# Kernel optimization log

Measured on AMD Instinct MI355X. Metric: run time of the kernel, lower is better.

## Reference

```python
import jax, jax.numpy as jnp
import numpy as np

NEG_SLOPE = 0.01  # torch F.leaky_relu default


def setup_inputs() -> dict:
    key = jax.random.key(0)
    k1, k2, k3, k4, k5 = jax.random.split(key, 5)
    N, E, IN_DIM, OUT_DIM = 100000, 1600000, 128, 64
    h = jax.random.normal(k1, (N, IN_DIM), dtype=jnp.float32)
    src = jax.random.randint(k2, (E,), 0, N, dtype=jnp.int64)
    dst = jax.random.randint(k3, (E,), 0, N, dtype=jnp.int64)
    # xavier_normal-ish scaled params
    W1 = jax.random.normal(k4, (OUT_DIM, IN_DIM), dtype=jnp.float32) * (2.0 / (IN_DIM + OUT_DIM)) ** 0.5
    Wa = jax.random.normal(k5, (1, 2 * OUT_DIM), dtype=jnp.float32) * (2.0 / (2 * OUT_DIM + 1)) ** 0.5
    return {"h": h, "src": src, "dst": dst, "W1": W1, "Wa": Wa}


def reference(h, src, dst, W1, Wa):
    N = h.shape[0]
    D = W1.shape[0]
    z = h @ W1.T  # [N, D]
    z_src = z[src]  # [E, D] gather
    z_dst = z[dst]  # [E, D] gather
    a_src, a_dst = Wa[0, :D], Wa[0, D:]
    # attn_fc(concat(z_src, z_dst)) == z_src@a_src + z_dst@a_dst
    e = z_src @ a_src + z_dst @ a_dst  # [E]
    e = jnp.where(e >= 0, e, NEG_SLOPE * e)  # leaky_relu
    # segment softmax over incoming edges of each dst node
    e_max = jax.ops.segment_max(e, dst, num_segments=N)
    e_max = jnp.where(jnp.isfinite(e_max), e_max, 0.0)  # empty segments
    e_exp = jnp.exp(e - e_max[dst])
    denom = jax.ops.segment_sum(e_exp, dst, num_segments=N)
    alpha = e_exp / jnp.maximum(denom, 1e-16)[dst]  # [E]
    # weighted scatter-sum of source messages
    h_out = jax.ops.segment_sum(alpha[:, None] * z_src, dst, num_segments=N)  # [N, D]
    return h_out
```

## Files before the change

### kernel.cpp

```cpp
#include <hip/hip_runtime.h>
#include <hip/hip_bf16.h>

#define NEG_SLOPE 0.01f
#define NPB 512
#define CHUNK 4096

typedef __attribute__((ext_vector_type(8))) short short8;
typedef __attribute__((ext_vector_type(4))) float f32x4;

__device__ __forceinline__ unsigned short f2bf_rne(float f) {
    unsigned u = __float_as_uint(f);
    u += 0x7FFFu + ((u >> 16) & 1u);
    return (unsigned short)(u >> 16);
}

__global__ __launch_bounds__(256, 4) void k_gp(
    const float* __restrict__ h, const float* __restrict__ W1,
    const float* __restrict__ Wa, unsigned short* __restrict__ zb,
    float* __restrict__ s, float* __restrict__ t, int N, int G1,
    const int* __restrict__ src, const int* __restrict__ dst,
    unsigned* __restrict__ gcur, unsigned* __restrict__ table,
    int E, int NBKT, int BCAP)
{
    __shared__ __align__(16) union SM {
        struct { short wsb[64 * 128]; short tbuf[4][16 * 64]; } g;
        struct {
            unsigned cnt[256]; unsigned exc[256]; unsigned sbuf[256];
            unsigned gbaseb[256]; unsigned stage[CHUNK];
            unsigned short bkt[CHUNK];
        } p;
    } sm;
    const int tid = threadIdx.x;

    if (blockIdx.x < (unsigned)G1) {
        const int nb = blockIdx.x * 256;
        const int w  = tid >> 6;
        const int l  = tid & 63;
        const int lr = l & 15;
        const int lc = l >> 4;
        const int rowbase = nb + w * 64;
        const float4* __restrict__ h4 = (const float4*)h;
        const float4* __restrict__ W14 = (const float4*)W1;

        float asrc[4], adst[4];
#pragma unroll
        for (int ni = 0; ni < 4; ++ni) {
            asrc[ni] = Wa[ni * 16 + lr];
            adst[ni] = Wa[64 + ni * 16 + lr];
        }

        float4 av[8];
        {
            const int myn = rowbase + lr;
#pragma unroll
            for (int ks = 0; ks < 4; ++ks) {
                const int kcb = ks * 4 + lc;
                if (myn < N) {
                    av[2 * ks]     = h4[(size_t)myn * 32 + kcb * 2];
                    av[2 * ks + 1] = h4[(size_t)myn * 32 + kcb * 2 + 1];
                } else {
                    av[2 * ks]     = make_float4(0.f, 0.f, 0.f, 0.f);
                    av[2 * ks + 1] = make_float4(0.f, 0.f, 0.f, 0.f);
                }
            }
        }

#pragma unroll
        for (int it = 0; it < 4; ++it) {
            const int q = tid + it * 256;
            const int r = q >> 4, cb = q & 15;
            float4 v0 = W14[(size_t)r * 32 + cb * 2];
            float4 v1 = W14[(size_t)r * 32 + cb * 2 + 1];
            short8 o;
            o[0]=f2bf_rne(v0.x); o[1]=f2bf_rne(v0.y); o[2]=f2bf_rne(v0.z); o[3]=f2bf_rne(v0.w);
            o[4]=f2bf_rne(v1.x); o[5]=f2bf_rne(v1.y); o[6]=f2bf_rne(v1.z); o[7]=f2bf_rne(v1.w);
            *(short8*)&sm.g.wsb[r * 128 + ((cb * 8) ^ ((r & 7) << 3))] = o;
        }
        __syncthreads();

        short* __restrict__ tb = sm.g.tbuf[w];

#pragma unroll
        for (int rg = 0; rg < 4; ++rg) {
            short8 afr[4];
#pragma unroll
            for (int ks = 0; ks < 4; ++ks) {
                const float4 v0 = av[2 * ks], v1 = av[2 * ks + 1];
                short8 o;
                o[0]=f2bf_rne(v0.x); o[1]=f2bf_rne(v0.y); o[2]=f2bf_rne(v0.z); o[3]=f2bf_rne(v0.w);
                o[4]=f2bf_rne(v1.x); o[5]=f2bf_rne(v1.y); o[6]=f2bf_rne(v1.z); o[7]=f2bf_rne(v1.w);
                afr[ks] = o;
            }
            if (rg < 3) {
                const int myn = rowbase + (rg + 1) * 16 + lr;
#pragma unroll
                for (int ks = 0; ks < 4; ++ks) {
                    const int kcb = ks * 4 + lc;
                    if (myn < N) {
                        av[2 * ks]     = h4[(size_t)myn * 32 + kcb * 2];
                        av[2 * ks + 1] = h4[(size_t)myn * 32 + kcb * 2 + 1];
                    } else {
                        av[2 * ks]     = make_float4(0.f, 0.f, 0.f, 0.f);
                        av[2 * ks + 1] = make_float4(0.f, 0.f, 0.f, 0.f);
                    }
                }
            }

            f32x4 acc[4];
#pragma unroll
            for (int ni = 0; ni < 4; ++ni) acc[ni] = (f32x4){0.f, 0.f, 0.f, 0.f};
#pragma unroll
            for (int ks = 0; ks < 4; ++ks) {
                const int kcb = ks * 4 + lc;
#pragma unroll
                for (int ni = 0; ni < 4; ++ni) {
                    const int wr = ni * 16 + lr;
                    const short8 bf = *(const short8*)&sm.g.wsb[wr * 128 + ((kcb * 8) ^ ((wr & 7) << 3))];
                    acc[ni] = __builtin_amdgcn_mfma_f32_16x16x32_bf16(afr[ks], bf, acc[ni], 0, 0, 0);
                }
            }

#pragma unroll
            for (int r = 0; r < 4; ++r) {
                float ps = 0.f, pt = 0.f;
#pragma unroll
                for (int ni = 0; ni < 4; ++ni) {
                    ps = fmaf(acc[ni][r], asrc[ni], ps);
                    pt = fmaf(acc[ni][r], adst[ni], pt);
                }
#pragma unroll
                for (int m = 1; m < 16; m <<= 1) {
                    ps += __shfl_xor(ps, m);
                    pt += __shfl_xor(pt, m);
                }
                const int node = rowbase + rg * 16 + lc * 4 + r;
                if (lr == 0 && node < N) { s[node] = ps; t[node] = pt; }
            }

#pragma unroll
            for (int ni = 0; ni < 4; ++ni) {
                const int col = ni * 16 + lr;
#pragma unroll
                for (int r = 0; r < 4; ++r) {
                    const int ro = lc * 4 + r;
                    tb[ro * 64 + (((col >> 3) ^ (ro & 7)) << 3) + (col & 7)]
                        = (short)f2bf_rne(acc[ni][r]);
                }
            }
            {
                const int ro = l >> 2;
                const int n = rowbase + rg * 16 + ro;
                if (n < N) {
#pragma unroll
                    for (int j = 0; j < 2; ++j) {
                        const int c = (l & 3) * 2 + j;
                        const short8 v = *(const short8*)&tb[ro * 64 + ((c ^ (ro & 7)) << 3)];
                        *(short8*)&zb[(size_t)n * 64 + c * 8] = v;
                    }
                }
            }
        }
    } else {
        const int e0 = (blockIdx.x - G1) * CHUNK;
        const int nE = min(CHUNK, E - e0);

        sm.p.cnt[tid] = 0u;
        __syncthreads();
        for (int i = tid; i < nE; i += 256)
            atomicAdd(&sm.p.cnt[(unsigned)dst[e0 + i] >> 9], 1u);
        __syncthreads();

        const unsigned myc = sm.p.cnt[tid];
        if (tid < NBKT && myc > 0u) sm.p.gbaseb[tid] = atomicAdd(&gcur[tid], myc);

        sm.p.sbuf[tid] = myc;
        __syncthreads();
        for (int off = 1; off < 256; off <<= 1) {
            unsigned x = (tid >= off) ? sm.p.sbuf[tid - off] : 0u;
            __syncthreads();
            sm.p.sbuf[tid] += x;
            __syncthreads();
        }
        sm.p.exc[tid] = sm.p.sbuf[tid] - myc;
        __syncthreads();
        sm.p.cnt[tid] = 0u;
        __syncthreads();

        for (int i = tid; i < nE; i += 256) {
            const unsigned d = (unsigned)dst[e0 + i];
            const unsigned b = d >> 9;
            const unsigned pos = sm.p.exc[b] + atomicAdd(&sm.p.cnt[b], 1u);
            sm.p.stage[pos] = ((unsigned)src[e0 + i] << 9) | (d & 511u);
            sm.p.bkt[pos] = (unsigned short)b;
        }
        __syncthreads();

        for (int i = tid; i < nE; i += 256) {
            const unsigned b = sm.p.bkt[i];
            const unsigned off = sm.p.gbaseb[b] + ((unsigned)i - sm.p.exc[b]);
            if (off < (unsigned)BCAP)
                table[(size_t)b * BCAP + off] = sm.p.stage[i];
        }
    }
}

__global__ __launch_bounds__(512) void k_sp(
    const unsigned* __restrict__ table, const unsigned* __restrict__ gcur,
    const float* __restrict__ s, const float* __restrict__ t,
    uint2* __restrict__ edge_ps, unsigned* __restrict__ offsets,
    unsigned* __restrict__ counts, float* __restrict__ invden,
    int N, int NBKT, int BCAP)
{
    __shared__ unsigned ncnt[NPB], nexc[NPB], scur[NPB], sbuf[NPB];
    __shared__ float tlds[NPB], den[NPB];
    __shared__ unsigned basesh;
    const int tid = threadIdx.x;
    const int b = blockIdx.x;
    const int bc = min((int)gcur[b], BCAP);
    const size_t tbo = (size_t)b * BCAP;
    const int node = b * NPB + tid;

    {
        unsigned c = (tid < NBKT) ? min(gcur[tid], (unsigned)BCAP) : 0u;
        sbuf[tid] = c;
        __syncthreads();
        for (int off = 1; off < NPB; off <<= 1) {
            unsigned x = (tid >= off) ? sbuf[tid - off] : 0u;
            __syncthreads();
            sbuf[tid] += x;
            __syncthreads();
        }
        if (tid == 0) basesh = (b == 0) ? 0u : sbuf[b - 1];
    }
    tlds[tid] = (node < N) ? t[node] : 0.f;
    den[tid] = 0.f;
    ncnt[tid] = 0u;
    __syncthreads();
    const unsigned base = basesh;

    for (int i = tid; i < bc; i += NPB)
        atomicAdd(&ncnt[table[tbo + i] & 511u], 1u);
    __syncthreads();

    const unsigned c0 = ncnt[tid];
    sbuf[tid] = c0;
    __syncthreads();
    for (int off = 1; off < NPB; off <<= 1) {
        unsigned x = (tid >= off) ? sbuf[tid - off] : 0u;
        __syncthreads();
        sbuf[tid] += x;
        __syncthreads();
    }
    nexc[tid] = sbuf[tid] - c0;
    scur[tid] = 0u;
    __syncthreads();

    if (node < N) { offsets[node] = base + nexc[tid]; counts[node] = c0; }

    for (int i = tid; i < bc; i += NPB) {
        const unsigned v = table[tbo + i];
        const unsigned l = v & 511u;
        const unsigned sj = v >> 9;
        float e = s[sj] + tlds[l];
        e = (e >= 0.f) ? e : NEG_SLOPE * e;
        const float p = __expf(e);
        const unsigned pos = nexc[l] + atomicAdd(&scur[l], 1u);
        edge_ps[base + pos] = make_uint2(__float_as_uint(p), sj);
        atomicAdd(&den[l], p);
    }
    __syncthreads();
    if (node < N) invden[node] = 1.f / fmaxf(den[tid], 1e-16f);
}

__global__ __launch_bounds__(256) void k_node(
    const unsigned* __restrict__ offsets, const unsigned* __restrict__ counts,
    const uint2* __restrict__ edge_ps, const float* __restrict__ invden,
    const unsigned short* __restrict__ zb, float* __restrict__ out, int N)
{
    const int tid = threadIdx.x;
    const int node = blockIdx.x * 16 + (tid >> 4);
    if (node >= N) return;
    const int wl    = tid & 63;
    const int gbase = wl & ~15;
    const int sub   = wl & 15;
    const int g2    = sub >> 3;
    const int l8    = sub & 7;

    const unsigned beg = offsets[node];
    const int cnt = (int)counts[node];
    if (cnt == 0) {
        if (sub < 8) {
            const float4 zz = make_float4(0.f, 0.f, 0.f, 0.f);
            *(float4*)&out[(size_t)node * 64 + sub * 8]     = zz;
            *(float4*)&out[(size_t)node * 64 + sub * 8 + 4] = zz;
        }
        return;
    }

    const float invd = invden[node];
    const unsigned short* __restrict__ zrow = zb + l8 * 8;
    float acc[8] = {0.f, 0.f, 0.f, 0.f, 0.f, 0.f, 0.f, 0.f};

    for (int base = 0; base < cnt; base += 16) {
        const int rem = cnt - base;
        uint2 ep = make_uint2(0u, 0u);
        if (sub < rem) ep = edge_ps[beg + base + sub];
        const float p = __uint_as_float(ep.x);
        const int  sj = (int)ep.y;

        uint4 vv[8];
#pragma unroll
        for (int k = 0; k < 8; ++k) {
            const int sjj = __shfl(sj, gbase + g2 * 8 + k);
            vv[k] = *(const uint4*)&zrow[(size_t)sjj * 64];
        }
#pragma unroll
        for (int k = 0; k < 8; ++k) {
            const float pj = __shfl(p, gbase + g2 * 8 + k);
            const uint4 v = vv[k];
#define UNPK(u, d0) \
            acc[d0]     = fmaf(pj, __uint_as_float((u) << 16),          acc[d0]); \
            acc[d0 + 1] = fmaf(pj, __uint_as_float((u) & 0xFFFF0000u), acc[d0 + 1]);
            UNPK(v.x, 0) UNPK(v.y, 2) UNPK(v.z, 4) UNPK(v.w, 6)
#undef UNPK
        }
    }

#pragma unroll
    for (int c = 0; c < 8; ++c)
        acc[c] += __shfl_xor(acc[c], 8);

    if (sub < 8) {
        float4 o0 = make_float4(acc[0] * invd, acc[1] * invd, acc[2] * invd, acc[3] * invd);
        float4 o1 = make_float4(acc[4] * invd, acc[5] * invd, acc[6] * invd, acc[7] * invd);
        *(float4*)&out[(size_t)node * 64 + sub * 8]     = o0;
        *(float4*)&out[(size_t)node * 64 + sub * 8 + 4] = o1;
    }
}

extern "C" void kernel_launch(void* const* d_in, const int* in_sizes, int n_in,
                              void* d_out, int out_size, void* d_ws, size_t ws_size,
                              hipStream_t stream) {
    const float* h   = (const float*)d_in[0];
    const int*   src = (const int*)d_in[1];
    const int*   dst = (const int*)d_in[2];
    const float* W1  = (const float*)d_in[3];
    const float* Wa  = (const float*)d_in[4];
    float* out = (float*)d_out;

    const int N = in_sizes[0] / 128;
    const int E = in_sizes[1];
    const int NBKT = (N + NPB - 1) / NPB;
    const int meanb = (E + NBKT - 1) / NBKT;
    int slack = 24 * (int)sqrtf((float)meanb) + 64;
    const int BCAP = meanb + slack;

    const int G1 = (N + 255) / 256;
    const int G2 = (E + CHUNK - 1) / CHUNK;

    unsigned short* zb = (unsigned short*)d_ws;
    float*    s        = (float*)(zb + (size_t)N * 64);
    float*    t        = s + N;
    unsigned* gcur     = (unsigned*)(t + N);
    unsigned* offsets  = gcur + NBKT;
    unsigned* counts   = offsets + N;
    float*    invden   = (float*)(counts + N);
    uint2*    edge_ps  = (uint2*)(invden + N);
    unsigned* table    = (unsigned*)(edge_ps + E);

    hipMemsetAsync(gcur, 0, (size_t)NBKT * sizeof(unsigned), stream);

    k_gp<<<G1 + G2, 256, 0, stream>>>(h, W1, Wa, zb, s, t, N, G1,
                                      src, dst, gcur, table, E, NBKT, BCAP);
    k_sp<<<NBKT, 512, 0, stream>>>(table, gcur, s, t, edge_ps, offsets, counts,
                                   invden, N, NBKT, BCAP);
    k_node<<<(N + 15) / 16, 256, 0, stream>>>(offsets, counts, edge_ps, invden, zb, out, N);
}
```

Before: 95.19 us.

## Fuse softmax and node aggregation into one kernel with LDS edge lists

Merges the per-bucket softmax kernel and the per-node aggregation kernel into one kernel. Each block handles a quarter of a 512-node bucket and keeps the sorted (p, src) edge list in shared memory, so the global edge_ps, offsets, counts and invden buffers and one launch go away. The cost is that every quarter-block rescans the whole bucket table (four times the table reads), and edges past QCAP are silently dropped. The bf16 conversion also switches to the library intrinsic, and the global prefix scan over buckets is no longer needed.

```diff
diff --git a/kernel.cpp b/kernel.cpp
--- a/kernel.cpp
+++ b/kernel.cpp
@@ -3,15 +3,35 @@
 
 #define NEG_SLOPE 0.01f
 #define NPB 512
+#define QN  128
+#define QCAP 2600
 #define CHUNK 4096
 
 typedef __attribute__((ext_vector_type(8))) short short8;
 typedef __attribute__((ext_vector_type(4))) float f32x4;
 
 __device__ __forceinline__ unsigned short f2bf_rne(float f) {
-    unsigned u = __float_as_uint(f);
-    u += 0x7FFFu + ((u >> 16) & 1u);
-    return (unsigned short)(u >> 16);
+    __hip_bfloat16 b = __float2bfloat16(f);
+    return __builtin_bit_cast(unsigned short, b);
+}
+
+__device__ __forceinline__ short8 cvt2(float4 v0, float4 v1) {
+    short8 o;
+    o[0]=(short)f2bf_rne(v0.x); o[1]=(short)f2bf_rne(v0.y);
+    o[2]=(short)f2bf_rne(v0.z); o[3]=(short)f2bf_rne(v0.w);
+    o[4]=(short)f2bf_rne(v1.x); o[5]=(short)f2bf_rne(v1.y);
+    o[6]=(short)f2bf_rne(v1.z); o[7]=(short)f2bf_rne(v1.w);
+    return o;
+}
+
+__device__ __forceinline__ unsigned wscan_incl(unsigned v) {
+    const int ln = threadIdx.x & 63;
+#pragma unroll
+    for (int off = 1; off < 64; off <<= 1) {
+        unsigned x = __shfl_up(v, off);
+        if (ln >= off) v += x;
+    }
+    return v;
 }
 
 __global__ __launch_bounds__(256, 4) void k_gp(
@@ -71,10 +91,7 @@
             const int r = q >> 4, cb = q & 15;
             float4 v0 = W14[(size_t)r * 32 + cb * 2];
             float4 v1 = W14[(size_t)r * 32 + cb * 2 + 1];
-            short8 o;
-            o[0]=f2bf_rne(v0.x); o[1]=f2bf_rne(v0.y); o[2]=f2bf_rne(v0.z); o[3]=f2bf_rne(v0.w);
-            o[4]=f2bf_rne(v1.x); o[5]=f2bf_rne(v1.y); o[6]=f2bf_rne(v1.z); o[7]=f2bf_rne(v1.w);
-            *(short8*)&sm.g.wsb[r * 128 + ((cb * 8) ^ ((r & 7) << 3))] = o;
+            *(short8*)&sm.g.wsb[r * 128 + ((cb * 8) ^ ((r & 7) << 3))] = cvt2(v0, v1);
         }
         __syncthreads();
 
@@ -84,13 +101,7 @@
         for (int rg = 0; rg < 4; ++rg) {
             short8 afr[4];
 #pragma unroll
-            for (int ks = 0; ks < 4; ++ks) {
-                const float4 v0 = av[2 * ks], v1 = av[2 * ks + 1];
-                short8 o;
-                o[0]=f2bf_rne(v0.x); o[1]=f2bf_rne(v0.y); o[2]=f2bf_rne(v0.z); o[3]=f2bf_rne(v0.w);
-                o[4]=f2bf_rne(v1.x); o[5]=f2bf_rne(v1.y); o[6]=f2bf_rne(v1.z); o[7]=f2bf_rne(v1.w);
-                afr[ks] = o;
-            }
+            for (int ks = 0; ks < 4; ++ks) afr[ks] = cvt2(av[2 * ks], av[2 * ks + 1]);
             if (rg < 3) {
                 const int myn = rowbase + (rg + 1) * 16 + lr;
 #pragma unroll
@@ -204,137 +215,117 @@
     }
 }
 
-__global__ __launch_bounds__(512) void k_sp(
+__global__ __launch_bounds__(256) void k_sn(
     const unsigned* __restrict__ table, const unsigned* __restrict__ gcur,
     const float* __restrict__ s, const float* __restrict__ t,
-    uint2* __restrict__ edge_ps, unsigned* __restrict__ offsets,
-    unsigned* __restrict__ counts, float* __restrict__ invden,
-    int N, int NBKT, int BCAP)
+    const unsigned short* __restrict__ zb, float* __restrict__ out,
+    int N, int BCAP)
 {
-    __shared__ unsigned ncnt[NPB], nexc[NPB], scur[NPB], sbuf[NPB];
-    __shared__ float tlds[NPB], den[NPB];
-    __shared__ unsigned basesh;
+    __shared__ unsigned ncnt[QN], nexc[QN], scur[QN];
+    __shared__ float tl[QN], den[QN], invd[QN];
+    __shared__ unsigned wtot[2];
+    __shared__ __align__(8) uint2 elist[QCAP];
+
     const int tid = threadIdx.x;
-    const int b = blockIdx.x;
+    const int b  = blockIdx.x >> 2;
+    const int qr = blockIdx.x & 3;
+    const int node0 = b * NPB + qr * QN;
     const int bc = min((int)gcur[b], BCAP);
     const size_t tbo = (size_t)b * BCAP;
-    const int node = b * NPB + tid;
-
-    {
-        unsigned c = (tid < NBKT) ? min(gcur[tid], (unsigned)BCAP) : 0u;
-        sbuf[tid] = c;
-        __syncthreads();
-        for (int off = 1; off < NPB; off <<= 1) {
-            unsigned x = (tid >= off) ? sbuf[tid - off] : 0u;
-            __syncthreads();
-            sbuf[tid] += x;
-            __syncthreads();
-        }
-        if (tid == 0) basesh = (b == 0) ? 0u : sbuf[b - 1];
-    }
-    tlds[tid] = (node < N) ? t[node] : 0.f;
-    den[tid] = 0.f;
-    ncnt[tid] = 0u;
-    __syncthreads();
-    const unsigned base = basesh;
-
-    for (int i = tid; i < bc; i += NPB)
-        atomicAdd(&ncnt[table[tbo + i] & 511u], 1u);
-    __syncthreads();
-
-    const unsigned c0 = ncnt[tid];
-    sbuf[tid] = c0;
-    __syncthreads();
-    for (int off = 1; off < NPB; off <<= 1) {
-        unsigned x = (tid >= off) ? sbuf[tid - off] : 0u;
-        __syncthreads();
-        sbuf[tid] += x;
-        __syncthreads();
-    }
-    nexc[tid] = sbuf[tid] - c0;
-    scur[tid] = 0u;
-    __syncthreads();
-
-    if (node < N) { offsets[node] = base + nexc[tid]; counts[node] = c0; }
-
-    for (int i = tid; i < bc; i += NPB) {
+
+    if (tid < QN) {
+        ncnt[tid] = 0u; scur[tid] = 0u; den[tid] = 0.f;
+        const int n = node0 + tid;
+        tl[tid] = (n < N) ? t[n] : 0.f;
+    }
+    __syncthreads();
+
+    for (int i = tid; i < bc; i += 256) {
         const unsigned v = table[tbo + i];
-        const unsigned l = v & 511u;
+        if (((v >> 7) & 3u) == (unsigned)qr)
+            atomicAdd(&ncnt[v & 127u], 1u);
+    }
+    __syncthreads();
+
+    if (tid < QN) {
+        const unsigned c = ncnt[tid];
+        const unsigned inc = wscan_incl(c);
+        if ((tid & 63) == 63) wtot[tid >> 6] = inc;
+        nexc[tid] = inc - c;
+    }
+    __syncthreads();
+    if (tid >= 64 && tid < QN) nexc[tid] += wtot[0];
+    __syncthreads();
+
+    for (int i = tid; i < bc; i += 256) {
+        const unsigned v = table[tbo + i];
+        if (((v >> 7) & 3u) != (unsigned)qr) continue;
+        const unsigned l = v & 127u;
         const unsigned sj = v >> 9;
-        float e = s[sj] + tlds[l];
+        float e = s[sj] + tl[l];
         e = (e >= 0.f) ? e : NEG_SLOPE * e;
         const float p = __expf(e);
         const unsigned pos = nexc[l] + atomicAdd(&scur[l], 1u);
-        edge_ps[base + pos] = make_uint2(__float_as_uint(p), sj);
-        atomicAdd(&den[l], p);
-    }
-    __syncthreads();
-    if (node < N) invden[node] = 1.f / fmaxf(den[tid], 1e-16f);
-}
-
-__global__ __launch_bounds__(256) void k_node(
-    const unsigned* __restrict__ offsets, const unsigned* __restrict__ counts,
-    const uint2* __restrict__ edge_ps, const float* __restrict__ invden,
-    const unsigned short* __restrict__ zb, float* __restrict__ out, int N)
-{
-    const int tid = threadIdx.x;
-    const int node = blockIdx.x * 16 + (tid >> 4);
-    if (node >= N) return;
+        if (pos < (unsigned)QCAP) {
+            elist[pos] = make_uint2(__float_as_uint(p), sj);
+            atomicAdd(&den[l], p);
+        }
+    }
+    __syncthreads();
+    if (tid < QN) invd[tid] = 1.f / fmaxf(den[tid], 1e-16f);
+    __syncthreads();
+
     const int wl    = tid & 63;
+    const int w     = tid >> 6;
     const int gbase = wl & ~15;
     const int sub   = wl & 15;
     const int g2    = sub >> 3;
     const int l8    = sub & 7;
-
-    const unsigned beg = offsets[node];
-    const int cnt = (int)counts[node];
-    if (cnt == 0) {
-        if (sub < 8) {
-            const float4 zz = make_float4(0.f, 0.f, 0.f, 0.f);
-            *(float4*)&out[(size_t)node * 64 + sub * 8]     = zz;
-            *(float4*)&out[(size_t)node * 64 + sub * 8 + 4] = zz;
-        }
-        return;
-    }
-
-    const float invd = invden[node];
     const unsigned short* __restrict__ zrow = zb + l8 * 8;
-    float acc[8] = {0.f, 0.f, 0.f, 0.f, 0.f, 0.f, 0.f, 0.f};
-
-    for (int base = 0; base < cnt; base += 16) {
-        const int rem = cnt - base;
-        uint2 ep = make_uint2(0u, 0u);
-        if (sub < rem) ep = edge_ps[beg + base + sub];
-        const float p = __uint_as_float(ep.x);
-        const int  sj = (int)ep.y;
-
-        uint4 vv[8];
-#pragma unroll
-        for (int k = 0; k < 8; ++k) {
-            const int sjj = __shfl(sj, gbase + g2 * 8 + k);
-            vv[k] = *(const uint4*)&zrow[(size_t)sjj * 64];
-        }
-#pragma unroll
-        for (int k = 0; k < 8; ++k) {
-            const float pj = __shfl(p, gbase + g2 * 8 + k);
-            const uint4 v = vv[k];
+
+    for (int grp = 0; grp < 8; ++grp) {
+        const int l  = grp * 16 + w * 4 + (wl >> 4);
+        const int gn = node0 + l;
+        const unsigned beg = nexc[l];
+        const int cnt = (int)ncnt[l];
+
+        float acc[8] = {0.f, 0.f, 0.f, 0.f, 0.f, 0.f, 0.f, 0.f};
+        for (int base = 0; base < cnt; base += 16) {
+            const int rem = cnt - base;
+            uint2 ep = make_uint2(0u, 0u);
+            if (sub < rem) ep = elist[beg + base + sub];
+            const float p = __uint_as_float(ep.x);
+            const int  sj = (int)ep.y;
+
+            uint4 vv[8];
+#pragma unroll
+            for (int k = 0; k < 8; ++k) {
+                const int sjj = __shfl(sj, gbase + g2 * 8 + k);
+                vv[k] = *(const uint4*)&zrow[(size_t)sjj * 64];
+            }
+#pragma unroll
+            for (int k = 0; k < 8; ++k) {
+                const float pj = __shfl(p, gbase + g2 * 8 + k);
+                const uint4 v = vv[k];
 #define UNPK(u, d0) \
-            acc[d0]     = fmaf(pj, __uint_as_float((u) << 16),          acc[d0]); \
-            acc[d0 + 1] = fmaf(pj, __uint_as_float((u) & 0xFFFF0000u), acc[d0 + 1]);
-            UNPK(v.x, 0) UNPK(v.y, 2) UNPK(v.z, 4) UNPK(v.w, 6)
+                acc[d0]     = fmaf(pj, __uint_as_float((u) << 16),          acc[d0]); \
+                acc[d0 + 1] = fmaf(pj, __uint_as_float((u) & 0xFFFF0000u), acc[d0 + 1]);
+                UNPK(v.x, 0) UNPK(v.y, 2) UNPK(v.z, 4) UNPK(v.w, 6)
 #undef UNPK
-        }
-    }
-
-#pragma unroll
-    for (int c = 0; c < 8; ++c)
-        acc[c] += __shfl_xor(acc[c], 8);
-
-    if (sub < 8) {
-        float4 o0 = make_float4(acc[0] * invd, acc[1] * invd, acc[2] * invd, acc[3] * invd);
-        float4 o1 = make_float4(acc[4] * invd, acc[5] * invd, acc[6] * invd, acc[7] * invd);
-        *(float4*)&out[(size_t)node * 64 + sub * 8]     = o0;
-        *(float4*)&out[(size_t)node * 64 + sub * 8 + 4] = o1;
+            }
+        }
+
+#pragma unroll
+        for (int c = 0; c < 8; ++c)
+            acc[c] += __shfl_xor(acc[c], 8);
+
+        if (sub < 8 && gn < N) {
+            const float iv = invd[l];
+            float4 o0 = make_float4(acc[0] * iv, acc[1] * iv, acc[2] * iv, acc[3] * iv);
+            float4 o1 = make_float4(acc[4] * iv, acc[5] * iv, acc[6] * iv, acc[7] * iv);
+            *(float4*)&out[(size_t)gn * 64 + sub * 8]     = o0;
+            *(float4*)&out[(size_t)gn * 64 + sub * 8 + 4] = o1;
+        }
     }
 }
 
@@ -362,17 +353,11 @@
     float*    s        = (float*)(zb + (size_t)N * 64);
     float*    t        = s + N;
     unsigned* gcur     = (unsigned*)(t + N);
-    unsigned* offsets  = gcur + NBKT;
-    unsigned* counts   = offsets + N;
-    float*    invden   = (float*)(counts + N);
-    uint2*    edge_ps  = (uint2*)(invden + N);
-    unsigned* table    = (unsigned*)(edge_ps + E);
+    unsigned* table    = gcur + NBKT;
 
     hipMemsetAsync(gcur, 0, (size_t)NBKT * sizeof(unsigned), stream);
 
     k_gp<<<G1 + G2, 256, 0, stream>>>(h, W1, Wa, zb, s, t, N, G1,
                                       src, dst, gcur, table, E, NBKT, BCAP);
-    k_sp<<<NBKT, 512, 0, stream>>>(table, gcur, s, t, edge_ps, offsets, counts,
-                                   invden, N, NBKT, BCAP);
-    k_node<<<(N + 15) / 16, 256, 0, stream>>>(offsets, counts, edge_ps, invden, zb, out, N);
-}
+    k_sn<<<NBKT * 4, 256, 0, stream>>>(table, gcur, s, t, zb, out, N, BCAP);
+}
```

Result: slower. 104.1 us (+9.3%).
